# Performance work log

Measured on AMD Instinct MI355X. Metric: run time of the kernel, lower is better.

The kernel has to match this reference:

```python
import math
import jax, jax.numpy as jnp
import numpy as np

# --- Configuration derived from init kwargs (mul=128, l=0..3, layout='mul_ir') ---
MUL = 128
B = 32768
IN_DIM = 2048   # 128*(1+3+5+7)
OUT_DIM = 2432  # 4*128 scalars + 128*(3+5+7)
# Each path: (in1_start, in2_start, out_start, w_start, mode, d)
# mode 0: l x l -> 0 (invariant contraction); mode 1: l x 0 -> l (scalar gating)
# in1/in2 slices: 0e@0(128), 1o@128(384), 2e@512(640), 3o@1152(896)
PATHS = [
    (0,    0,    0,    0 * MUL * MUL, 0, 1),   # 0e x 0e -> 0e
    (128,  128,  128,  1 * MUL * MUL, 0, 3),   # 1o x 1o -> 0e
    (512,  512,  256,  2 * MUL * MUL, 0, 5),   # 2e x 2e -> 0e
    (1152, 1152, 384,  3 * MUL * MUL, 0, 7),   # 3o x 3o -> 0e
    (128,  0,    512,  4 * MUL * MUL, 1, 3),   # 1o x 0e -> 1o
    (512,  0,    896,  5 * MUL * MUL, 1, 5),   # 2e x 0e -> 2e
    (1152, 0,    1536, 6 * MUL * MUL, 1, 7),   # 3o x 0e -> 3o
]
W_NUMEL = 7 * MUL * MUL  # 114688


def setup_inputs() -> dict:
    key = jax.random.key(0)
    k1, k2, k3 = jax.random.split(key, 3)
    x1 = jax.random.normal(k1, (B, IN_DIM), dtype=jnp.float32)
    x2 = jax.random.normal(k2, (B, IN_DIM), dtype=jnp.float32)
    weight = jax.random.normal(k3, (W_NUMEL,), dtype=jnp.float32)
    output_mask = jnp.ones((OUT_DIM,), dtype=jnp.float32)
    return {"x1": x1, "x2": x2, "weight": weight, "output_mask": output_mask}


def reference(x1, x2, weight, output_mask):
    batch = x1.shape[0]
    out = jnp.zeros((batch, OUT_DIM), dtype=x1.dtype)
    for in1s, in2s, outs, ws, mode, d in PATHS:
        w = weight[ws:ws + MUL * MUL].reshape(MUL, MUL)  # [u, v]
        inv_sqrt_d = 1.0 / math.sqrt(float(d))
        x1v = x1[:, in1s:in1s + MUL * d].reshape(batch, MUL, d)  # [b, u, d]
        if mode == 0:
            # l x l -> 0: einsum('bud,bvd->buv')/sqrt(d) then 'buv,uv->bu'.
            # Contract v with w first to avoid the [b,u,v] intermediate.
            x2v = x2[:, in2s:in2s + MUL * d].reshape(batch, MUL, d)  # [b, v, d]
            tmp = jnp.einsum('bvd,uv->bud', x2v, w)
            mixed = jnp.sum(x1v * tmp, axis=2) * inv_sqrt_d  # [b, u]
            out = out.at[:, outs:outs + MUL].add(mixed)
        else:
            # l x 0 -> l: scalar gating. path_weight folded as 1.0.
            scalars = x2[:, in2s:in2s + MUL]  # [b, v]
            mixed = jnp.einsum('bv,uv->bu', scalars, w)  # [b, u]
            contrib = x1v * mixed[:, :, None] * inv_sqrt_d  # [b, u, d]
            out = out.at[:, outs:outs + MUL * d].add(contrib.reshape(batch, MUL * d))
    return out * output_mask
```

## Files before the change

### kernel.cpp

```cpp
#include <hip/hip_runtime.h>
#include <stdint.h>


#define IN_DIM 2048
#define OUT_DIM 2432
#define TB 16
#define SROW 136
#define PLANE 2184
#define TPAD 129

using bf16x8 = __attribute__((ext_vector_type(8))) short;
using f32x4  = __attribute__((ext_vector_type(4))) float;

__device__ __forceinline__ short f2bf(float f) {
  uint32_t u = __float_as_uint(f);
  uint32_t r = (u + 0x7fffu + ((u >> 16) & 1u)) >> 16;
  return (short)r;
}

__device__ __forceinline__ bf16x8 pack8(float4 lo, float4 hi) {
  bf16x8 r;
  r[0] = f2bf(lo.x); r[1] = f2bf(lo.y); r[2] = f2bf(lo.z); r[3] = f2bf(lo.w);
  r[4] = f2bf(hi.x); r[5] = f2bf(hi.y); r[6] = f2bf(hi.z); r[7] = f2bf(hi.w);
  return r;
}

template <int D, bool HASM1>
__device__ __forceinline__ void run_group(
    const float* __restrict__ x1, const float* __restrict__ x2,
    const float* __restrict__ w, const float* __restrict__ mask,
    float* __restrict__ out,
    int tile, int rs, int outs0, int w0off, int outs1, int w1off, float inv,
    short* x2s, short* scal, float* tmp, float* mixed1)
{
  const int t   = threadIdx.x;
  const int L   = t & 63;
  const int wid = t >> 6;
  const int l16 = L & 15;
  const int kg  = L >> 4;
  const int b0  = tile * TB;

  for (int i = t; i < TB * 128 * D; i += 256) {
    int b  = i / (128 * D);
    int c  = i - b * (128 * D);
    int v  = c / D;
    int dd = c - v * D;
    float val = x2[(size_t)(b0 + b) * IN_DIM + rs + c];
    x2s[dd * PLANE + b * SROW + v] = f2bf(val);
  }
  if (HASM1) {
    for (int i = t; i < TB * 128; i += 256) {
      int b = i >> 7, v = i & 127;
      scal[b * SROW + v] = f2bf(x2[(size_t)(b0 + b) * IN_DIM + v]);
    }
  }
  __syncthreads();

  if (HASM1) {
    bf16x8 a4[4];
#pragma unroll
    for (int k = 0; k < 4; k++)
      a4[k] = *(const bf16x8*)&scal[l16 * SROW + kg * 8 + k * 32];
#pragma unroll
    for (int ti = 0; ti < 2; ti++) {
      int ut = (wid * 2 + ti) * 16 + l16;
      f32x4 acc = {0.f, 0.f, 0.f, 0.f};
#pragma unroll
      for (int k = 0; k < 4; k++) {
        const float4* p = (const float4*)(w + w1off + ut * 128 + kg * 8 + k * 32);
        bf16x8 bf = pack8(p[0], p[1]);
        acc = __builtin_amdgcn_mfma_f32_16x16x32_bf16(a4[k], bf, acc, 0, 0, 0);
      }
#pragma unroll
      for (int r = 0; r < 4; r++)
        mixed1[(kg * 4 + r) * TPAD + (wid * 2 + ti) * 16 + l16] = acc[r];
    }
  }

  bf16x8 w0f[2][4];
#pragma unroll
  for (int ti = 0; ti < 2; ti++) {
    int ut = (wid * 2 + ti) * 16 + l16;
#pragma unroll
    for (int k = 0; k < 4; k++) {
      const float4* p = (const float4*)(w + w0off + ut * 128 + kg * 8 + k * 32);
      w0f[ti][k] = pack8(p[0], p[1]);
    }
  }

  const int uu = t & 127;
  const int hb = t >> 7;
  float m0acc[8];
#pragma unroll
  for (int i = 0; i < 8; i++) m0acc[i] = 0.f;

  for (int dd = 0; dd < D; dd++) {
    float xv[8];
#pragma unroll
    for (int i = 0; i < 8; i++) {
      int b = 2 * i + hb;
      xv[i] = x1[(size_t)(b0 + b) * IN_DIM + rs + uu * D + dd];
    }

    bf16x8 bfr[4];
#pragma unroll
    for (int k = 0; k < 4; k++)
      bfr[k] = *(const bf16x8*)&x2s[dd * PLANE + l16 * SROW + kg * 8 + k * 32];
#pragma unroll
    for (int ti = 0; ti < 2; ti++) {
      f32x4 acc = {0.f, 0.f, 0.f, 0.f};
#pragma unroll
      for (int k = 0; k < 4; k++)
        acc = __builtin_amdgcn_mfma_f32_16x16x32_bf16(w0f[ti][k], bfr[k], acc, 0, 0, 0);
#pragma unroll
      for (int r = 0; r < 4; r++)
        tmp[l16 * TPAD + (wid * 2 + ti) * 16 + kg * 4 + r] = acc[r];
    }
    __syncthreads();

#pragma unroll
    for (int i = 0; i < 8; i++) {
      int b = 2 * i + hb;
      m0acc[i] += xv[i] * tmp[b * TPAD + uu];
    }
    __syncthreads();
  }

  {
    float mk0 = mask[outs0 + uu] * inv;
#pragma unroll
    for (int i = 0; i < 8; i++) {
      int b = 2 * i + hb;
      out[(size_t)(b0 + b) * OUT_DIM + outs0 + uu] = m0acc[i] * mk0;
    }
  }

  if (HASM1) {
    float mkv[D];
#pragma unroll
    for (int dd = 0; dd < D; dd++) mkv[dd] = mask[outs1 + uu * D + dd] * inv;
#pragma unroll
    for (int i = 0; i < 8; i++) {
      int b = 2 * i + hb;
      float m1 = mixed1[b * TPAD + uu];
#pragma unroll
      for (int dd = 0; dd < D; dd++) {
        float xv = x1[(size_t)(b0 + b) * IN_DIM + rs + uu * D + dd];
        out[(size_t)(b0 + b) * OUT_DIM + outs1 + uu * D + dd] = xv * m1 * mkv[dd];
      }
    }
  }
}

__global__ void __launch_bounds__(256, 3)
tp_kernel(const float* __restrict__ x1, const float* __restrict__ x2,
          const float* __restrict__ w, const float* __restrict__ mask,
          float* __restrict__ out)
{
  __shared__ __align__(16) short x2s[7 * PLANE];
  __shared__ __align__(16) short scal[TB * SROW];
  __shared__ __align__(16) float tmp[TB * TPAD];
  __shared__ __align__(16) float mixed1[TB * TPAD];

  int bx   = blockIdx.x;
  int g    = bx & 3;
  int tile = bx >> 2;

  switch (g) {
    case 0:
      run_group<1, false>(x1, x2, w, mask, out, tile, 0, 0, 0 * 16384, 0, 0,
                          1.0f, x2s, scal, tmp, mixed1);
      break;
    case 1:
      run_group<3, true>(x1, x2, w, mask, out, tile, 128, 128, 1 * 16384, 512, 4 * 16384,
                         0.5773502691896258f, x2s, scal, tmp, mixed1);
      break;
    case 2:
      run_group<5, true>(x1, x2, w, mask, out, tile, 512, 256, 2 * 16384, 896, 5 * 16384,
                         0.4472135954999579f, x2s, scal, tmp, mixed1);
      break;
    case 3:
      run_group<7, true>(x1, x2, w, mask, out, tile, 1152, 384, 3 * 16384, 1536, 6 * 16384,
                         0.3779644730092272f, x2s, scal, tmp, mixed1);
      break;
  }
}

extern "C" void kernel_launch(void* const* d_in, const int* in_sizes, int n_in,
                              void* d_out, int out_size, void* d_ws, size_t ws_size,
                              hipStream_t stream) {
  const float* x1   = (const float*)d_in[0];
  const float* x2   = (const float*)d_in[1];
  const float* w    = (const float*)d_in[2];
  const float* mask = (const float*)d_in[3];
  float* out = (float*)d_out;

  dim3 grid(4 * (32768 / TB));
  dim3 block(256);
  tp_kernel<<<grid, block, 0, stream>>>(x1, x2, w, mask, out);
}
```

Before: 946.4 us.

## Fuse x1 dot product into MFMA accumulator registers, drop tmp shared buffer

The invariant contraction no longer writes MFMA results into a shared tmp buffer and rereads them after two barriers per d. Each lane now multiplies its MFMA accumulator elements directly by register-held x1 values matching its (batch, u) fragment positions. Those x1 values are loaded once and reused for the gated l x 0 output, which removes the second global read of x1. The cost is 4*D floats per lane in registers, which raises register pressure for D=7. The global accesses also change shape: each lane reads contiguous x1 runs per batch row and writes scattered outputs.

```diff
diff --git a/kernel.cpp b/kernel.cpp
--- a/kernel.cpp
+++ b/kernel.cpp
@@ -31,7 +31,7 @@
     const float* __restrict__ w, const float* __restrict__ mask,
     float* __restrict__ out,
     int tile, int rs, int outs0, int w0off, int outs1, int w1off, float inv,
-    short* x2s, short* scal, float* tmp, float* mixed1)
+    short* x2s, short* scal, float* mixed1)
 {
   const int t   = threadIdx.x;
   const int L   = t & 63;
@@ -75,78 +75,57 @@
       for (int r = 0; r < 4; r++)
         mixed1[(kg * 4 + r) * TPAD + (wid * 2 + ti) * 16 + l16] = acc[r];
     }
+    __syncthreads();
   }
 
-  bf16x8 w0f[2][4];
 #pragma unroll
   for (int ti = 0; ti < 2; ti++) {
-    int ut = (wid * 2 + ti) * 16 + l16;
+    const int ut = (wid * 2 + ti) * 16 + l16;
+    const int u0 = (wid * 2 + ti) * 16 + kg * 4;
+
+    bf16x8 w0f[4];
 #pragma unroll
     for (int k = 0; k < 4; k++) {
       const float4* p = (const float4*)(w + w0off + ut * 128 + kg * 8 + k * 32);
-      w0f[ti][k] = pack8(p[0], p[1]);
-    }
-  }
-
-  const int uu = t & 127;
-  const int hb = t >> 7;
-  float m0acc[8];
-#pragma unroll
-  for (int i = 0; i < 8; i++) m0acc[i] = 0.f;
-
-  for (int dd = 0; dd < D; dd++) {
-    float xv[8];
-#pragma unroll
-    for (int i = 0; i < 8; i++) {
-      int b = 2 * i + hb;
-      xv[i] = x1[(size_t)(b0 + b) * IN_DIM + rs + uu * D + dd];
+      w0f[k] = pack8(p[0], p[1]);
     }
 
-    bf16x8 bfr[4];
+    const float* xrow = x1 + (size_t)(b0 + l16) * IN_DIM + rs + u0 * D;
+    float xv[4 * D];
 #pragma unroll
-    for (int k = 0; k < 4; k++)
-      bfr[k] = *(const bf16x8*)&x2s[dd * PLANE + l16 * SROW + kg * 8 + k * 32];
+    for (int n = 0; n < 4 * D; n++) xv[n] = xrow[n];
+
+    f32x4 m0acc = {0.f, 0.f, 0.f, 0.f};
 #pragma unroll
-    for (int ti = 0; ti < 2; ti++) {
+    for (int dd = 0; dd < D; dd++) {
+      bf16x8 bfr[4];
+#pragma unroll
+      for (int k = 0; k < 4; k++)
+        bfr[k] = *(const bf16x8*)&x2s[dd * PLANE + l16 * SROW + kg * 8 + k * 32];
       f32x4 acc = {0.f, 0.f, 0.f, 0.f};
 #pragma unroll
       for (int k = 0; k < 4; k++)
-        acc = __builtin_amdgcn_mfma_f32_16x16x32_bf16(w0f[ti][k], bfr[k], acc, 0, 0, 0);
+        acc = __builtin_amdgcn_mfma_f32_16x16x32_bf16(w0f[k], bfr[k], acc, 0, 0, 0);
 #pragma unroll
       for (int r = 0; r < 4; r++)
-        tmp[l16 * TPAD + (wid * 2 + ti) * 16 + kg * 4 + r] = acc[r];
+        m0acc[r] += acc[r] * xv[r * D + dd];
     }
-    __syncthreads();
+
+    const size_t orow = (size_t)(b0 + l16) * OUT_DIM;
 
 #pragma unroll
-    for (int i = 0; i < 8; i++) {
-      int b = 2 * i + hb;
-      m0acc[i] += xv[i] * tmp[b * TPAD + uu];
-    }
-    __syncthreads();
-  }
+    for (int r = 0; r < 4; r++)
+      out[orow + outs0 + u0 + r] = m0acc[r] * inv * mask[outs0 + u0 + r];
 
-  {
-    float mk0 = mask[outs0 + uu] * inv;
+    if (HASM1) {
 #pragma unroll
-    for (int i = 0; i < 8; i++) {
-      int b = 2 * i + hb;
-      out[(size_t)(b0 + b) * OUT_DIM + outs0 + uu] = m0acc[i] * mk0;
-    }
-  }
-
-  if (HASM1) {
-    float mkv[D];
+      for (int r = 0; r < 4; r++) {
+        float m1 = mixed1[l16 * TPAD + u0 + r];
 #pragma unroll
-    for (int dd = 0; dd < D; dd++) mkv[dd] = mask[outs1 + uu * D + dd] * inv;
-#pragma unroll
-    for (int i = 0; i < 8; i++) {
-      int b = 2 * i + hb;
-      float m1 = mixed1[b * TPAD + uu];
-#pragma unroll
-      for (int dd = 0; dd < D; dd++) {
-        float xv = x1[(size_t)(b0 + b) * IN_DIM + rs + uu * D + dd];
-        out[(size_t)(b0 + b) * OUT_DIM + outs1 + uu * D + dd] = xv * m1 * mkv[dd];
+        for (int dd = 0; dd < D; dd++) {
+          int col = outs1 + (u0 + r) * D + dd;
+          out[orow + col] = xv[r * D + dd] * m1 * inv * mask[col];
+        }
       }
     }
   }
@@ -159,7 +138,6 @@
 {
   __shared__ __align__(16) short x2s[7 * PLANE];
   __shared__ __align__(16) short scal[TB * SROW];
-  __shared__ __align__(16) float tmp[TB * TPAD];
   __shared__ __align__(16) float mixed1[TB * TPAD];
 
   int bx   = blockIdx.x;
@@ -169,19 +147,19 @@
   switch (g) {
     case 0:
       run_group<1, false>(x1, x2, w, mask, out, tile, 0, 0, 0 * 16384, 0, 0,
-                          1.0f, x2s, scal, tmp, mixed1);
+                          1.0f, x2s, scal, mixed1);
       break;
     case 1:
       run_group<3, true>(x1, x2, w, mask, out, tile, 128, 128, 1 * 16384, 512, 4 * 16384,
-                         0.5773502691896258f, x2s, scal, tmp, mixed1);
+                         0.5773502691896258f, x2s, scal, mixed1);
       break;
     case 2:
       run_group<5, true>(x1, x2, w, mask, out, tile, 512, 256, 2 * 16384, 896, 5 * 16384,
-                         0.4472135954999579f, x2s, scal, tmp, mixed1);
+                         0.4472135954999579f, x2s, scal, mixed1);
       break;
     case 3:
       run_group<7, true>(x1, x2, w, mask, out, tile, 1152, 384, 3 * 16384, 1536, 6 * 16384,
-                         0.3779644730092272f, x2s, scal, tmp, mixed1);
+                         0.3779644730092272f, x2s, scal, mixed1);
       break;
   }
 }
```

New measurement: 994.5 us. +5.1%, slower.
